# Kernel tuning notes

Hardware: AMD Instinct MI355X
Metric: run time of the kernel (lower is better)

## Reference

```python
import jax, jax.numpy as jnp
import numpy as np

B, C, H = 8, 768, 12
TH = TW = 16
SH = SW = 32
N = TH * TW + SH * SW  # 1280


def setup_inputs() -> dict:
    key = jax.random.key(0)
    k1, k2, k3 = jax.random.split(key, 3)
    return {
        "x": jax.random.normal(k1, (B, N, C), jnp.float32),
        "qkv_w": jax.random.normal(k2, (3 * C, C), jnp.float32) * 0.02,
        "proj_w": jax.random.normal(k3, (C, C), jnp.float32) * 0.02,
        "proj_b": jnp.zeros((C,), jnp.float32),
        "t_h": TH, "t_w": TW, "s_h": SH, "s_w": SW,
    }


def reference(x, qkv_w, proj_w, proj_b, t_h, t_w, s_h, s_w):
    Bb, Nn, Cc = x.shape
    hd = Cc // H
    scale = hd ** -0.5
    nt = t_h * t_w
    ns = s_h * s_w
    # qkv projection: torch Linear computes x @ W.T
    qkv = (x @ qkv_w.T).reshape(Bb, Nn, 3, H, hd).transpose(2, 0, 3, 1, 4)
    q, k, v = qkv[0], qkv[1], qkv[2]  # each [B, H, N, hd]
    q_mt, q_s = q[:, :, :nt], q[:, :, nt:]
    k_mt, v_mt = k[:, :, :nt], v[:, :, :nt]
    # template queries attend only to template keys
    attn_t = jax.nn.softmax(jnp.einsum('bhqd,bhkd->bhqk', q_mt, k_mt) * scale, axis=-1)
    x_mt = jnp.einsum('bhqk,bhkd->bhqd', attn_t, v_mt).transpose(0, 2, 1, 3).reshape(Bb, nt, Cc)
    # search queries attend to all (template + search) keys
    attn_s = jax.nn.softmax(jnp.einsum('bhqd,bhkd->bhqk', q_s, k) * scale, axis=-1)
    x_s = jnp.einsum('bhqk,bhkd->bhqd', attn_s, v).transpose(0, 2, 1, 3).reshape(Bb, ns, Cc)
    out = jnp.concatenate([x_mt, x_s], axis=1)
    out = out @ proj_w.T + proj_b
    return out
```

## Files before the change

kernel.cpp:

```cpp
#include <hip/hip_runtime.h>
#include <hip/hip_bf16.h>


typedef __attribute__((ext_vector_type(8))) short s8v;
typedef __attribute__((ext_vector_type(4))) float f4v;
typedef __attribute__((ext_vector_type(4))) unsigned short u4v;
typedef __attribute__((ext_vector_type(4))) unsigned int u4i;
typedef __attribute__((ext_vector_type(2))) unsigned int u2i;

#define MFMA16(a, b, c) __builtin_amdgcn_mfma_f32_16x16x32_bf16((a), (b), (c), 0, 0, 0)

#define QSCALE 0.1803368801f

__device__ __forceinline__ unsigned short f2bf(float f) {
  unsigned int u = __builtin_bit_cast(unsigned int, f);
  u += 0x7fffu + ((u >> 16) & 1u);
  return (unsigned short)(u >> 16);
}

__device__ __forceinline__ unsigned int pk2(float lo, float hi) {
  __hip_bfloat162 t = __float22bfloat162_rn(make_float2(lo, hi));
  unsigned int u;
  __builtin_memcpy(&u, &t, 4);
  return u;
}

__device__ __forceinline__ s8v pack8(const float* p0, const float* p1) {
  u4i pi;
  pi[0] = pk2(p0[0], p0[1]);
  pi[1] = pk2(p0[2], p0[3]);
  pi[2] = pk2(p1[0], p1[1]);
  pi[3] = pk2(p1[2], p1[3]);
  return __builtin_bit_cast(s8v, pi);
}

__global__ __launch_bounds__(256) void cvt3_kernel(const float* __restrict__ x,
                                                   const float* __restrict__ wq,
                                                   const float* __restrict__ wp,
                                                   unsigned short* __restrict__ xb,
                                                   unsigned short* __restrict__ wqb,
                                                   unsigned short* __restrict__ wpb) {
  int i = blockIdx.x * 256 + threadIdx.x;
  const float* src;
  unsigned short* dst;
  int j;
  if (i < 1966080) {
    src = x; dst = xb; j = i;
  } else if (i < 1966080 + 442368) {
    src = wq; dst = wqb; j = i - 1966080;
  } else {
    src = wp; dst = wpb; j = i - (1966080 + 442368);
  }
  f4v v = ((const f4v*)src)[j];
  u4v o;
  o[0] = f2bf(v[0]); o[1] = f2bf(v[1]); o[2] = f2bf(v[2]); o[3] = f2bf(v[3]);
  ((u4v*)dst)[j] = o;
}


#define GEMM_STAGE(AS, BS, kt_)                                                             \
  do {                                                                                      \
    __builtin_amdgcn_global_load_lds(                                                       \
        (const __attribute__((address_space(1))) unsigned int*)(gA0 + (kt_)),               \
        (__attribute__((address_space(3))) unsigned int*)((char*)(AS) + tid * 16), 16, 0, 0); \
    __builtin_amdgcn_global_load_lds(                                                       \
        (const __attribute__((address_space(1))) unsigned int*)(gB0 + (kt_)),               \
        (__attribute__((address_space(3))) unsigned int*)((char*)(BS) + tid * 16), 16, 0, 0); \
    __builtin_amdgcn_global_load_lds(                                                       \
        (const __attribute__((address_space(1))) unsigned int*)(gA1 + (kt_)),               \
        (__attribute__((address_space(3))) unsigned int*)((char*)(AS) + (256 + tid) * 16),  \
        16, 0, 0);                                                                          \
    __builtin_amdgcn_global_load_lds(                                                       \
        (const __attribute__((address_space(1))) unsigned int*)(gB1 + (kt_)),               \
        (__attribute__((address_space(3))) unsigned int*)((char*)(BS) + (256 + tid) * 16),  \
        16, 0, 0);                                                                          \
  } while (0)

#define PIPE_WAIT4(cond_more)                                                               \
  do {                                                                                      \
    if (cond_more) asm volatile("s_waitcnt vmcnt(4) lgkmcnt(0)" ::: "memory");              \
    else           asm volatile("s_waitcnt vmcnt(0) lgkmcnt(0)" ::: "memory");              \
    __builtin_amdgcn_s_barrier();                                                           \
    __builtin_amdgcn_sched_barrier(0);                                                      \
  } while (0)

__global__ __launch_bounds__(256) void gemm_qkv_kernel(
    const unsigned short* __restrict__ A,
    const unsigned short* __restrict__ Bm,
    unsigned short* __restrict__ qb, unsigned short* __restrict__ kb,
    unsigned short* __restrict__ vT) {
  const int K = 768;
  __shared__ __align__(16) unsigned short As[3][128 * 32];
  __shared__ __align__(16) unsigned short Bs[3][128 * 32];
  int tid = threadIdx.x;
  int wave = tid >> 6, lane = tid & 63;
  int quad = lane >> 4, l16 = lane & 15;
  int wm = wave >> 1, wn = wave & 1;
  int l = blockIdx.x;
  int xcd = l & 7;
  int idx = l >> 3;
  int by = xcd * 10 + idx / 18;
  int bxg = idx - (idx / 18) * 18;
  int m0 = by * 128, n0 = bxg * 128;

  int srow = tid >> 2;
  int scol = (((tid & 3) ^ ((tid >> 3) & 3)) << 3);
  const unsigned short* gA0 = A + (size_t)(m0 + srow) * K + scol;
  const unsigned short* gA1 = A + (size_t)(m0 + srow + 64) * K + scol;
  const unsigned short* gB0 = Bm + (size_t)(n0 + srow) * K + scol;
  const unsigned short* gB1 = Bm + (size_t)(n0 + srow + 64) * K + scol;

  int rquad = quad ^ ((l16 >> 1) & 3);

  f4v acc[4][4];
#pragma unroll
  for (int i = 0; i < 4; ++i)
#pragma unroll
    for (int j = 0; j < 4; ++j) acc[i][j] = (f4v){0.f, 0.f, 0.f, 0.f};

  GEMM_STAGE(As[0], Bs[0], 0);
  GEMM_STAGE(As[1], Bs[1], 32);

  int bfc = 0, bfs = 2;
  for (int t = 0; t < 24; ++t) {
    PIPE_WAIT4(t + 1 < 24);
    if (t + 2 < 24) GEMM_STAGE(As[bfs], Bs[bfs], (t + 2) * 32);

    const unsigned short* Ab = As[bfc];
    const unsigned short* Bb = Bs[bfc];
    s8v af[4], bfr[4];
#pragma unroll
    for (int mi = 0; mi < 4; ++mi)
      af[mi] = *(const s8v*)&Ab[(wm * 64 + mi * 16 + l16) * 32 + rquad * 8];
#pragma unroll
    for (int ni = 0; ni < 4; ++ni)
      bfr[ni] = *(const s8v*)&Bb[(wn * 64 + ni * 16 + l16) * 32 + rquad * 8];
#pragma unroll
    for (int mi = 0; mi < 4; ++mi)
#pragma unroll
      for (int ni = 0; ni < 4; ++ni)
        acc[mi][ni] = MFMA16(af[mi], bfr[ni], acc[mi][ni]);

    bfc = (bfc == 2) ? 0 : bfc + 1;
    bfs = (bfs == 2) ? 0 : bfs + 1;
  }

  int which = n0 / 768;
  if (which == 2) {
#pragma unroll
    for (int ni = 0; ni < 4; ++ni) {
      int oo = n0 + wn * 64 + ni * 16 + l16 - 1536;
      int hh = oo >> 6;
      int dd = oo & 63;
#pragma unroll
      for (int mi = 0; mi < 4; ++mi) {
        int gm = m0 + wm * 64 + mi * 16 + quad * 4;
        int bb = gm / 1280;
        int nn = gm - bb * 1280;
        u2i w;
        w[0] = pk2(acc[mi][ni][0], acc[mi][ni][1]);
        w[1] = pk2(acc[mi][ni][2], acc[mi][ni][3]);
        *(u2i*)(vT + (((size_t)bb * 12 + hh) * 64 + dd) * 1280 + nn) = w;
      }
    }
  } else {
    unsigned short* dst = which ? kb : qb;
    float sc = which ? 1.0f : QSCALE;
#pragma unroll
    for (int ni = 0; ni < 4; ++ni) {
      int oo = n0 + wn * 64 + ni * 16 + l16 - which * 768;
      int hh = oo >> 6;
      int dd = oo & 63;
#pragma unroll
      for (int mi = 0; mi < 4; ++mi) {
#pragma unroll
        for (int r = 0; r < 4; ++r) {
          int gm = m0 + wm * 64 + mi * 16 + quad * 4 + r;
          int bb = gm / 1280;
          int nn = gm - bb * 1280;
          dst[(((size_t)bb * 12 + hh) * 1280 + nn) * 64 + dd] = f2bf(acc[mi][ni][r] * sc);
        }
      }
    }
  }
}

__global__ __launch_bounds__(256) void gemm_proj_kernel(
    const unsigned short* __restrict__ A,
    const unsigned short* __restrict__ Bm,
    const float* __restrict__ pb, float* __restrict__ out) {
  const int K = 768;
  __shared__ __align__(16) unsigned short As[3][128 * 32];
  __shared__ __align__(16) unsigned short Bs[3][128 * 32];
  int tid = threadIdx.x;
  int wave = tid >> 6, lane = tid & 63;
  int quad = lane >> 4, l16 = lane & 15;
  int wm = wave >> 1, wn = wave & 1;
  int l = blockIdx.x;
  int xcd = l & 7;
  int idx = l >> 3;
  int by = xcd * 10 + idx / 6;
  int bxg = idx - (idx / 6) * 6;
  int m0 = by * 128, n0 = bxg * 128;

  int srow = tid >> 2;
  int scol = (((tid & 3) ^ ((tid >> 3) & 3)) << 3);
  const unsigned short* gA0 = A + (size_t)(m0 + srow) * K + scol;
  const unsigned short* gA1 = A + (size_t)(m0 + srow + 64) * K + scol;
  const unsigned short* gB0 = Bm + (size_t)(n0 + srow) * K + scol;
  const unsigned short* gB1 = Bm + (size_t)(n0 + srow + 64) * K + scol;

  int rquad = quad ^ ((l16 >> 1) & 3);

  f4v acc[4][4];
#pragma unroll
  for (int i = 0; i < 4; ++i)
#pragma unroll
    for (int j = 0; j < 4; ++j) acc[i][j] = (f4v){0.f, 0.f, 0.f, 0.f};

  GEMM_STAGE(As[0], Bs[0], 0);
  GEMM_STAGE(As[1], Bs[1], 32);

  int bfc = 0, bfs = 2;
  for (int t = 0; t < 24; ++t) {
    PIPE_WAIT4(t + 1 < 24);
    if (t + 2 < 24) GEMM_STAGE(As[bfs], Bs[bfs], (t + 2) * 32);

    const unsigned short* Ab = As[bfc];
    const unsigned short* Bb = Bs[bfc];
    s8v af[4], bfr[4];
#pragma unroll
    for (int mi = 0; mi < 4; ++mi)
      af[mi] = *(const s8v*)&Ab[(wm * 64 + mi * 16 + l16) * 32 + rquad * 8];
#pragma unroll
    for (int ni = 0; ni < 4; ++ni)
      bfr[ni] = *(const s8v*)&Bb[(wn * 64 + ni * 16 + l16) * 32 + rquad * 8];
#pragma unroll
    for (int mi = 0; mi < 4; ++mi)
#pragma unroll
      for (int ni = 0; ni < 4; ++ni)
        acc[mi][ni] = MFMA16(af[mi], bfr[ni], acc[mi][ni]);

    bfc = (bfc == 2) ? 0 : bfc + 1;
    bfs = (bfs == 2) ? 0 : bfs + 1;
  }

#pragma unroll
  for (int ni = 0; ni < 4; ++ni) {
    int gn = n0 + wn * 64 + ni * 16 + l16;
    float bias = pb[gn];
#pragma unroll
    for (int mi = 0; mi < 4; ++mi)
#pragma unroll
      for (int r = 0; r < 4; ++r) {
        int gm = m0 + wm * 64 + mi * 16 + quad * 4 + r;
        out[(size_t)gm * 768 + gn] = acc[mi][ni][r] + bias;
      }
  }
}

__global__ __launch_bounds__(256) void attn_kernel(
    const unsigned short* __restrict__ qb, const unsigned short* __restrict__ kb,
    const unsigned short* __restrict__ vT, unsigned short* __restrict__ attnb) {
  const int NT = 1280, CC = 768;
  int l = blockIdx.x;
  int xcd = l & 7;
  int idx = l >> 3;
  int grp = xcd * 12 + idx / 10;
  int bx = idx - (idx / 10) * 10;
  int b = grp / 12;
  int h = grp - b * 12;
  int nk, qstart;
  if (bx < 8) { nk = 1280; qstart = 256 + bx * 128; }
  else        { nk = 256;  qstart = (bx - 8) * 128; }
  int wave = threadIdx.x >> 6, lane = threadIdx.x & 63;
  int quad = lane >> 4, l16 = lane & 15;
  int qa = qstart + wave * 32;
  int ntiles = nk >> 6;

  const unsigned short* qp = qb + (((size_t)b * 12 + h) * NT + qa) * 64;
  const unsigned short* kp = kb + (((size_t)b * 12 + h) * NT) * 64;
  const unsigned short* vp = vT + (((size_t)b * 12 + h) * 64) * NT;

  __shared__ __align__(16) unsigned short Kl[3][8][512];
  __shared__ __align__(16) unsigned short Vl[3][8][512];

  s8v bq0 = *(const s8v*)(qp + l16 * 64 + quad * 8);
  s8v bq1 = *(const s8v*)(qp + l16 * 64 + 32 + quad * 8);
  s8v bq2 = *(const s8v*)(qp + (16 + l16) * 64 + quad * 8);
  s8v bq3 = *(const s8v*)(qp + (16 + l16) * 64 + 32 + quad * 8);

  int perm = ((l16 >> 2) << 3) + (l16 & 3);
  int f0 = wave * 2, f1 = wave * 2 + 1;
  int koffs0, koffs1, voffs0, voffs1;
  {
    int s = f0 >> 2, dh = (f0 >> 1) & 1, hh = f0 & 1;
    koffs0 = (s * 32 + hh * 4 + perm) * 64 + (dh * 4 + quad) * 8;
    s = f1 >> 2; dh = (f1 >> 1) & 1; hh = f1 & 1;
    koffs1 = (s * 32 + hh * 4 + perm) * 64 + (dh * 4 + quad) * 8;
    int dt = f0 >> 1, sv = f0 & 1;
    voffs0 = (dt * 16 + l16) * NT + sv * 32 + quad * 8;
    dt = f1 >> 1; sv = f1 & 1;
    voffs1 = (dt * 16 + l16) * NT + sv * 32 + quad * 8;
  }

#define STAGE(bfi, k0_)                                                                     \
  do {                                                                                      \
    __builtin_amdgcn_global_load_lds(                                                       \
        (const __attribute__((address_space(1))) unsigned int*)(kp + (size_t)(k0_)*64 +     \
                                                                koffs0),                    \
        (__attribute__((address_space(3))) unsigned int*)((char*)&Kl[bfi][f0][0] +          \
                                                          lane * 16),                       \
        16, 0, 0);                                                                          \
    __builtin_amdgcn_global_load_lds(                                                       \
        (const __attribute__((address_space(1))) unsigned int*)(kp + (size_t)(k0_)*64 +     \
                                                                koffs1),                    \
        (__attribute__((address_space(3))) unsigned int*)((char*)&Kl[bfi][f1][0] +          \
                                                          lane * 16),                       \
        16, 0, 0);                                                                          \
    __builtin_amdgcn_global_load_lds(                                                       \
        (const __attribute__((address_space(1))) unsigned int*)(vp + (size_t)(k0_) +        \
                                                                voffs0),                    \
        (__attribute__((address_space(3))) unsigned int*)((char*)&Vl[bfi][f0][0] +          \
                                                          lane * 16),                       \
        16, 0, 0);                                                                          \
    __builtin_amdgcn_global_load_lds(                                                       \
        (const __attribute__((address_space(1))) unsigned int*)(vp + (size_t)(k0_) +        \
                                                                voffs1),                    \
        (__attribute__((address_space(3))) unsigned int*)((char*)&Vl[bfi][f1][0] +          \
                                                          lane * 16),                       \
        16, 0, 0);                                                                          \
  } while (0)

  float la = 0.f, lb = 0.f;
  f4v Oa[4], Ob[4];
#pragma unroll
  for (int dt = 0; dt < 4; ++dt) {
    Oa[dt] = (f4v){0.f, 0.f, 0.f, 0.f};
    Ob[dt] = (f4v){0.f, 0.f, 0.f, 0.f};
  }

  STAGE(0, 0);
  STAGE(1, 64);

  int bfc = 0, bfs = 2;
  for (int t = 0; t < ntiles; ++t) {
    PIPE_WAIT4(t + 1 < ntiles);
    if (t + 2 < ntiles) STAGE(bfs, (t + 2) * 64);

    s8v kf[8];
#pragma unroll
    for (int ff = 0; ff < 8; ++ff) kf[ff] = *(const s8v*)&Kl[bfc][ff][lane * 8];

#pragma unroll
    for (int s = 0; s < 2; ++s) {
      int s4 = s << 2;
      f4v s0a = {0.f, 0.f, 0.f, 0.f}, s1a = {0.f, 0.f, 0.f, 0.f};
      f4v s0b = {0.f, 0.f, 0.f, 0.f}, s1b = {0.f, 0.f, 0.f, 0.f};
      __builtin_amdgcn_s_setprio(1);
      s0a = MFMA16(kf[s4 | 0], bq0, s0a);
      s0a = MFMA16(kf[s4 | 2], bq1, s0a);
      s1a = MFMA16(kf[s4 | 1], bq0, s1a);
      s1a = MFMA16(kf[s4 | 3], bq1, s1a);
      s0b = MFMA16(kf[s4 | 0], bq2, s0b);
      s0b = MFMA16(kf[s4 | 2], bq3, s0b);
      s1b = MFMA16(kf[s4 | 1], bq2, s1b);
      s1b = MFMA16(kf[s4 | 3], bq3, s1b);
      __builtin_amdgcn_s_setprio(0);

      float p0a[4], p1a[4], p0b[4], p1b[4];
#pragma unroll
      for (int r = 0; r < 4; ++r) {
        p0a[r] = __builtin_amdgcn_exp2f(s0a[r]);
        p1a[r] = __builtin_amdgcn_exp2f(s1a[r]);
        p0b[r] = __builtin_amdgcn_exp2f(s0b[r]);
        p1b[r] = __builtin_amdgcn_exp2f(s1b[r]);
      }
      la += ((p0a[0] + p0a[1]) + (p0a[2] + p0a[3])) + ((p1a[0] + p1a[1]) + (p1a[2] + p1a[3]));
      lb += ((p0b[0] + p0b[1]) + (p0b[2] + p0b[3])) + ((p1b[0] + p1b[1]) + (p1b[2] + p1b[3]));

      s8v pa = pack8(p0a, p1a);
      s8v pbv = pack8(p0b, p1b);

      s8v vf[4];
#pragma unroll
      for (int dt = 0; dt < 4; ++dt) vf[dt] = *(const s8v*)&Vl[bfc][dt * 2 + s][lane * 8];
      __builtin_amdgcn_s_setprio(1);
#pragma unroll
      for (int dt = 0; dt < 4; ++dt) {
        Oa[dt] = MFMA16(vf[dt], pa, Oa[dt]);
        Ob[dt] = MFMA16(vf[dt], pbv, Ob[dt]);
      }
      __builtin_amdgcn_s_setprio(0);
    }

    bfc = (bfc == 2) ? 0 : bfc + 1;
    bfs = (bfs == 2) ? 0 : bfs + 1;
  }
#undef STAGE

  la += __shfl_xor(la, 16, 64);
  la += __shfl_xor(la, 32, 64);
  lb += __shfl_xor(lb, 16, 64);
  lb += __shfl_xor(lb, 32, 64);
  float inva = 1.f / la, invb = 1.f / lb;

  size_t rowa = ((size_t)b * NT + qa + l16) * CC + h * 64;
  size_t rowb = ((size_t)b * NT + qa + 16 + l16) * CC + h * 64;
#pragma unroll
  for (int dt = 0; dt < 4; ++dt) {
    u4v ova, ovb;
#pragma unroll
    for (int r = 0; r < 4; ++r) {
      ova[r] = f2bf(Oa[dt][r] * inva);
      ovb[r] = f2bf(Ob[dt][r] * invb);
    }
    *(u4v*)(attnb + rowa + dt * 16 + quad * 4) = ova;
    *(u4v*)(attnb + rowb + dt * 16 + quad * 4) = ovb;
  }
}

extern "C" void kernel_launch(void* const* d_in, const int* in_sizes, int n_in,
                              void* d_out, int out_size, void* d_ws, size_t ws_size,
                              hipStream_t stream) {
  const float* x = (const float*)d_in[0];
  const float* qkv_w = (const float*)d_in[1];
  const float* proj_w = (const float*)d_in[2];
  const float* proj_b = (const float*)d_in[3];
  float* out = (float*)d_out;

  char* ws = (char*)d_ws;
  unsigned short* xb = (unsigned short*)(ws + 0);
  unsigned short* wqkvb = (unsigned short*)(ws + 15728640);
  unsigned short* wpb = (unsigned short*)(ws + 19267584);
  unsigned short* qb = (unsigned short*)(ws + 20447232);
  unsigned short* kbuf = (unsigned short*)(ws + 36175872);
  unsigned short* vT = (unsigned short*)(ws + 51904512);
  unsigned short* attnb = xb;

  cvt3_kernel<<<dim3(9984), 256, 0, stream>>>(x, qkv_w, proj_w, xb, wqkvb, wpb);

  gemm_qkv_kernel<<<dim3(1440), 256, 0, stream>>>(xb, wqkvb, qb, kbuf, vT);
  attn_kernel<<<dim3(960), 256, 0, stream>>>(qb, kbuf, vT, attnb);
  gemm_proj_kernel<<<dim3(480), 256, 0, stream>>>(attnb, wpb, proj_b, out);
}
```

Before: 247.5 us.

## Load K/V fragments directly from global into registers, drop LDS staging

Replaces the triple-buffered LDS pipeline (global_load_lds plus barrier waits) with direct per-wave global loads of K and V fragments into registers. A two-slot register double buffer over 32-key chunks prefetches the next chunk while the current one runs its MFMAs. This removes LDS traffic and block-level synchronisation. In exchange, the four waves of a block no longer share K/V loads, so global/L2 traffic rises roughly fourfold, and register pressure goes up.

Result: slower. 331.9 us (+34.1%).

```diff
diff --git a/kernel.cpp b/kernel.cpp
--- a/kernel.cpp
+++ b/kernel.cpp
@@ -276,14 +276,11 @@
   int wave = threadIdx.x >> 6, lane = threadIdx.x & 63;
   int quad = lane >> 4, l16 = lane & 15;
   int qa = qstart + wave * 32;
-  int ntiles = nk >> 6;
+  int nch = nk >> 5;
 
   const unsigned short* qp = qb + (((size_t)b * 12 + h) * NT + qa) * 64;
   const unsigned short* kp = kb + (((size_t)b * 12 + h) * NT) * 64;
   const unsigned short* vp = vT + (((size_t)b * 12 + h) * 64) * NT;
-
-  __shared__ __align__(16) unsigned short Kl[3][8][512];
-  __shared__ __align__(16) unsigned short Vl[3][8][512];
 
   s8v bq0 = *(const s8v*)(qp + l16 * 64 + quad * 8);
   s8v bq1 = *(const s8v*)(qp + l16 * 64 + 32 + quad * 8);
@@ -291,45 +288,66 @@
   s8v bq3 = *(const s8v*)(qp + (16 + l16) * 64 + 32 + quad * 8);
 
   int perm = ((l16 >> 2) << 3) + (l16 & 3);
-  int f0 = wave * 2, f1 = wave * 2 + 1;
-  int koffs0, koffs1, voffs0, voffs1;
-  {
-    int s = f0 >> 2, dh = (f0 >> 1) & 1, hh = f0 & 1;
-    koffs0 = (s * 32 + hh * 4 + perm) * 64 + (dh * 4 + quad) * 8;
-    s = f1 >> 2; dh = (f1 >> 1) & 1; hh = f1 & 1;
-    koffs1 = (s * 32 + hh * 4 + perm) * 64 + (dh * 4 + quad) * 8;
-    int dt = f0 >> 1, sv = f0 & 1;
-    voffs0 = (dt * 16 + l16) * NT + sv * 32 + quad * 8;
-    dt = f1 >> 1; sv = f1 & 1;
-    voffs1 = (dt * 16 + l16) * NT + sv * 32 + quad * 8;
-  }
-
-#define STAGE(bfi, k0_)                                                                     \
+  int ko0 = (perm) * 64 + (quad) * 8;
+  int ko1 = (4 + perm) * 64 + (quad) * 8;
+  int ko2 = (perm) * 64 + (4 + quad) * 8;
+  int ko3 = (4 + perm) * 64 + (4 + quad) * 8;
+  int vo0 = (l16) * NT + quad * 8;
+  int vo1 = (16 + l16) * NT + quad * 8;
+  int vo2 = (32 + l16) * NT + quad * 8;
+  int vo3 = (48 + l16) * NT + quad * 8;
+
+#define LOADT(kf, vf, k0_)                                                                  \
   do {                                                                                      \
-    __builtin_amdgcn_global_load_lds(                                                       \
-        (const __attribute__((address_space(1))) unsigned int*)(kp + (size_t)(k0_)*64 +     \
-                                                                koffs0),                    \
-        (__attribute__((address_space(3))) unsigned int*)((char*)&Kl[bfi][f0][0] +          \
-                                                          lane * 16),                       \
-        16, 0, 0);                                                                          \
-    __builtin_amdgcn_global_load_lds(                                                       \
-        (const __attribute__((address_space(1))) unsigned int*)(kp + (size_t)(k0_)*64 +     \
-                                                                koffs1),                    \
-        (__attribute__((address_space(3))) unsigned int*)((char*)&Kl[bfi][f1][0] +          \
-                                                          lane * 16),                       \
-        16, 0, 0);                                                                          \
-    __builtin_amdgcn_global_load_lds(                                                       \
-        (const __attribute__((address_space(1))) unsigned int*)(vp + (size_t)(k0_) +        \
-                                                                voffs0),                    \
-        (__attribute__((address_space(3))) unsigned int*)((char*)&Vl[bfi][f0][0] +          \
-                                                          lane * 16),                       \
-        16, 0, 0);                                                                          \
-    __builtin_amdgcn_global_load_lds(                                                       \
-        (const __attribute__((address_space(1))) unsigned int*)(vp + (size_t)(k0_) +        \
-                                                                voffs1),                    \
-        (__attribute__((address_space(3))) unsigned int*)((char*)&Vl[bfi][f1][0] +          \
-                                                          lane * 16),                       \
-        16, 0, 0);                                                                          \
+    const unsigned short* kc = kp + (size_t)(k0_)*64;                                       \
+    const unsigned short* vc = vp + (k0_);                                                  \
+    kf##0 = *(const s8v*)(kc + ko0);                                                        \
+    kf##1 = *(const s8v*)(kc + ko1);                                                        \
+    kf##2 = *(const s8v*)(kc + ko2);                                                        \
+    kf##3 = *(const s8v*)(kc + ko3);                                                        \
+    vf##0 = *(const s8v*)(vc + vo0);                                                        \
+    vf##1 = *(const s8v*)(vc + vo1);                                                        \
+    vf##2 = *(const s8v*)(vc + vo2);                                                        \
+    vf##3 = *(const s8v*)(vc + vo3);                                                        \
+  } while (0)
+
+#define CHUNK(kf, vf)                                                                       \
+  do {                                                                                      \
+    f4v s0a = {0.f, 0.f, 0.f, 0.f}, s1a = {0.f, 0.f, 0.f, 0.f};                             \
+    f4v s0b = {0.f, 0.f, 0.f, 0.f}, s1b = {0.f, 0.f, 0.f, 0.f};                             \
+    __builtin_amdgcn_s_setprio(1);                                                          \
+    s0a = MFMA16(kf##0, bq0, s0a);                                                          \
+    s0a = MFMA16(kf##2, bq1, s0a);                                                          \
+    s1a = MFMA16(kf##1, bq0, s1a);                                                          \
+    s1a = MFMA16(kf##3, bq1, s1a);                                                          \
+    s0b = MFMA16(kf##0, bq2, s0b);                                                          \
+    s0b = MFMA16(kf##2, bq3, s0b);                                                          \
+    s1b = MFMA16(kf##1, bq2, s1b);                                                          \
+    s1b = MFMA16(kf##3, bq3, s1b);                                                          \
+    __builtin_amdgcn_s_setprio(0);                                                          \
+    float p0a[4], p1a[4], p0b[4], p1b[4];                                                   \
+    _Pragma("unroll") for (int r = 0; r < 4; ++r) {                                         \
+      p0a[r] = __builtin_amdgcn_exp2f(s0a[r]);                                              \
+      p1a[r] = __builtin_amdgcn_exp2f(s1a[r]);                                              \
+      p0b[r] = __builtin_amdgcn_exp2f(s0b[r]);                                              \
+      p1b[r] = __builtin_amdgcn_exp2f(s1b[r]);                                              \
+    }                                                                                       \
+    la += ((p0a[0] + p0a[1]) + (p0a[2] + p0a[3])) +                                         \
+          ((p1a[0] + p1a[1]) + (p1a[2] + p1a[3]));                                          \
+    lb += ((p0b[0] + p0b[1]) + (p0b[2] + p0b[3])) +                                         \
+          ((p1b[0] + p1b[1]) + (p1b[2] + p1b[3]));                                          \
+    s8v pa = pack8(p0a, p1a);                                                               \
+    s8v pbv = pack8(p0b, p1b);                                                              \
+    __builtin_amdgcn_s_setprio(1);                                                          \
+    Oa[0] = MFMA16(vf##0, pa, Oa[0]);                                                       \
+    Ob[0] = MFMA16(vf##0, pbv, Ob[0]);                                                      \
+    Oa[1] = MFMA16(vf##1, pa, Oa[1]);                                                       \
+    Ob[1] = MFMA16(vf##1, pbv, Ob[1]);                                                      \
+    Oa[2] = MFMA16(vf##2, pa, Oa[2]);                                                       \
+    Ob[2] = MFMA16(vf##2, pbv, Ob[2]);                                                      \
+    Oa[3] = MFMA16(vf##3, pa, Oa[3]);                                                       \
+    Ob[3] = MFMA16(vf##3, pbv, Ob[3]);                                                      \
+    __builtin_amdgcn_s_setprio(0);                                                          \
   } while (0)
 
   float la = 0.f, lb = 0.f;
@@ -340,64 +358,19 @@
     Ob[dt] = (f4v){0.f, 0.f, 0.f, 0.f};
   }
 
-  STAGE(0, 0);
-  STAGE(1, 64);
-
-  int bfc = 0, bfs = 2;
-  for (int t = 0; t < ntiles; ++t) {
-    PIPE_WAIT4(t + 1 < ntiles);
-    if (t + 2 < ntiles) STAGE(bfs, (t + 2) * 64);
-
-    s8v kf[8];
-#pragma unroll
-    for (int ff = 0; ff < 8; ++ff) kf[ff] = *(const s8v*)&Kl[bfc][ff][lane * 8];
-
-#pragma unroll
-    for (int s = 0; s < 2; ++s) {
-      int s4 = s << 2;
-      f4v s0a = {0.f, 0.f, 0.f, 0.f}, s1a = {0.f, 0.f, 0.f, 0.f};
-      f4v s0b = {0.f, 0.f, 0.f, 0.f}, s1b = {0.f, 0.f, 0.f, 0.f};
-      __builtin_amdgcn_s_setprio(1);
-      s0a = MFMA16(kf[s4 | 0], bq0, s0a);
-      s0a = MFMA16(kf[s4 | 2], bq1, s0a);
-      s1a = MFMA16(kf[s4 | 1], bq0, s1a);
-      s1a = MFMA16(kf[s4 | 3], bq1, s1a);
-      s0b = MFMA16(kf[s4 | 0], bq2, s0b);
-      s0b = MFMA16(kf[s4 | 2], bq3, s0b);
-      s1b = MFMA16(kf[s4 | 1], bq2, s1b);
-      s1b = MFMA16(kf[s4 | 3], bq3, s1b);
-      __builtin_amdgcn_s_setprio(0);
-
-      float p0a[4], p1a[4], p0b[4], p1b[4];
-#pragma unroll
-      for (int r = 0; r < 4; ++r) {
-        p0a[r] = __builtin_amdgcn_exp2f(s0a[r]);
-        p1a[r] = __builtin_amdgcn_exp2f(s1a[r]);
-        p0b[r] = __builtin_amdgcn_exp2f(s0b[r]);
-        p1b[r] = __builtin_amdgcn_exp2f(s1b[r]);
-      }
-      la += ((p0a[0] + p0a[1]) + (p0a[2] + p0a[3])) + ((p1a[0] + p1a[1]) + (p1a[2] + p1a[3]));
-      lb += ((p0b[0] + p0b[1]) + (p0b[2] + p0b[3])) + ((p1b[0] + p1b[1]) + (p1b[2] + p1b[3]));
-
-      s8v pa = pack8(p0a, p1a);
-      s8v pbv = pack8(p0b, p1b);
-
-      s8v vf[4];
-#pragma unroll
-      for (int dt = 0; dt < 4; ++dt) vf[dt] = *(const s8v*)&Vl[bfc][dt * 2 + s][lane * 8];
-      __builtin_amdgcn_s_setprio(1);
-#pragma unroll
-      for (int dt = 0; dt < 4; ++dt) {
-        Oa[dt] = MFMA16(vf[dt], pa, Oa[dt]);
-        Ob[dt] = MFMA16(vf[dt], pbv, Ob[dt]);
-      }
-      __builtin_amdgcn_s_setprio(0);
-    }
-
-    bfc = (bfc == 2) ? 0 : bfc + 1;
-    bfs = (bfs == 2) ? 0 : bfs + 1;
-  }
-#undef STAGE
+  s8v kA0, kA1, kA2, kA3, vA0, vA1, vA2, vA3;
+  s8v kB0, kB1, kB2, kB3, vB0, vB1, vB2, vB3;
+
+  LOADT(kA, vA, 0);
+#pragma unroll 1
+  for (int t = 0; t < nch; t += 2) {
+    LOADT(kB, vB, (t + 1) * 32);
+    CHUNK(kA, vA);
+    if (t + 2 < nch) LOADT(kA, vA, (t + 2) * 32);
+    CHUNK(kB, vB);
+  }
+#undef LOADT
+#undef CHUNK
 
   la += __shfl_xor(la, 16, 64);
   la += __shfl_xor(la, 32, 64);
```
